# Kernel optimization log

Hardware: AMD Instinct MI355X
Metric: run time of the kernel (lower is better)

## Reference

```python
import jax, jax.numpy as jnp
import numpy as np

T, D, E, DFF, TOPK = 32768, 1024, 8, 2048, 2


def setup_inputs() -> dict:
    key = jax.random.key(0)
    k1, k2, k3, k4 = jax.random.split(key, 4)
    x = jax.random.normal(k1, (T, D), dtype=jnp.float32)
    gating_output = jax.random.normal(k2, (T, E), dtype=jnp.float32)
    # gate_up_proj: [E, 2*d_ff, d] (gate rows then up rows, col-parallel concat)
    w13 = jax.random.normal(k3, (E, 2 * DFF, D), dtype=jnp.float32) * 0.02
    # down_proj: [E, d, d_ff] (torch Linear weight layout)
    w2 = jax.random.normal(k4, (E, D, DFF), dtype=jnp.float32) * 0.02
    return {"x": x, "gating_output": gating_output, "w13": w13, "w2": w2, "topk": TOPK}


def reference(x, gating_output, w13, w2, topk):
    n_tok, d = x.shape
    n_exp = w13.shape[0]
    d_ff = w2.shape[2]
    # router: softmax over experts in fp32, top-k, renormalize, cast to x dtype
    probs = jax.nn.softmax(gating_output.astype(jnp.float32), axis=1)
    rw, sel = jax.lax.top_k(probs, topk)          # [T, topk]
    rw = rw / jnp.sum(rw, axis=-1, keepdims=True)
    rw = rw.astype(x.dtype)
    # dense combine weights [T, E] (zeros except selected experts)
    combine = jnp.zeros((n_tok, n_exp), dtype=x.dtype)
    combine = combine.at[jnp.arange(n_tok)[:, None], sel].set(rw)
    out = jnp.zeros_like(x)
    for e in range(n_exp):  # static small loop over experts
        gu = x @ w13[e].T                          # [T, 2*d_ff]
        g, u = gu[:, :d_ff], gu[:, d_ff:]
        h = jax.nn.silu(g) * u                     # [T, d_ff]
        out = out + combine[:, e:e + 1] * (h @ w2[e].T)
    return out
```

## Files before the change

### kernel.cpp

```cpp
#include <hip/hip_runtime.h>
#include <stdint.h>

#define T_TOK 32768
#define DIM   1024
#define NEXP  8
#define DFFN  2048
#define MAXROWS 67584
#define NBLK  128
#define NT1 16
#define NT2 32

typedef __bf16 bf16x8 __attribute__((ext_vector_type(8)));
typedef float  f32x4  __attribute__((ext_vector_type(4)));
typedef unsigned short u16x8 __attribute__((ext_vector_type(8)));

__device__ __forceinline__ unsigned short f2bf(float f) {
  unsigned u = __float_as_uint(f);
  unsigned r = (u + 0x7fffu + ((u >> 16) & 1u)) >> 16;
  return (unsigned short)r;
}
__device__ __forceinline__ float bf2f(unsigned short u) {
  return __uint_as_float(((unsigned)u) << 16);
}

__device__ __forceinline__ void gload16(const void* g, void* l) {
  __builtin_amdgcn_global_load_lds(
      (__attribute__((address_space(1))) void*)(uintptr_t)g,
      (__attribute__((address_space(3))) void*)(uint32_t)(uintptr_t)l,
      16, 0, 0);
}

__device__ __forceinline__ void xcd_remap(int NX, int NY, int& nb, int& mb) {
  int orig = blockIdx.y * NX + blockIdx.x;
  int q = (NX * NY) >> 3;
  int wgid = (orig & 7) * q + (orig >> 3);
  mb = wgid / NX;
  nb = wgid % NX;
}

__global__ void route_kernel(const float* __restrict__ gating, int* __restrict__ sel,
                             float* __restrict__ selw, int* __restrict__ blockHist) {
  __shared__ int hist[NEXP];
  const int tid = threadIdx.x;
  if (tid < NEXP) hist[tid] = 0;
  __syncthreads();
  int t = blockIdx.x * 256 + tid;
  float4 a = ((const float4*)gating)[t * 2];
  float4 b = ((const float4*)gating)[t * 2 + 1];
  float l[8] = {a.x, a.y, a.z, a.w, b.x, b.y, b.z, b.w};
  int i0 = 0; float b0 = l[0];
#pragma unroll
  for (int i = 1; i < 8; ++i) if (l[i] > b0) { b0 = l[i]; i0 = i; }
  int i1 = -1; float b1 = -1e30f;
#pragma unroll
  for (int i = 0; i < 8; ++i) if (i != i0 && l[i] > b1) { b1 = l[i]; i1 = i; }
  float e1 = __expf(b1 - b0);
  float w0 = 1.f / (1.f + e1);
  float w1 = 1.f - w0;
  sel[2 * t] = i0;  sel[2 * t + 1] = i1;
  selw[2 * t] = w0; selw[2 * t + 1] = w1;
  atomicAdd(&hist[i0], 1);
  atomicAdd(&hist[i1], 1);
  __syncthreads();
  if (tid < NEXP) blockHist[blockIdx.x * NEXP + tid] = hist[tid];
}

__global__ void plan_kernel(const int* __restrict__ blockHist,
                            int* __restrict__ padOff, int* __restrict__ base) {
  __shared__ int totals[NEXP];
  const int tid = threadIdx.x;
  if (tid < NEXP) {
    int s = 0;
    for (int b = 0; b < NBLK; ++b) s += blockHist[b * NEXP + tid];
    totals[tid] = s;
  }
  __syncthreads();
  if (tid == 0) {
    int off = 0;
    for (int e = 0; e < NEXP; ++e) { padOff[e] = off; off += (totals[e] + 255) & ~255; }
    padOff[NEXP] = off;
  }
  if (tid < NEXP) {
    int off = 0;
    for (int e = 0; e < tid; ++e) off += (totals[e] + 255) & ~255;
    int run = off;
    for (int b = 0; b < NBLK; ++b) { base[b * NEXP + tid] = run; run += blockHist[b * NEXP + tid]; }
  }
}

__global__ void fill_kernel(int* __restrict__ rowTok, int* __restrict__ rowSlot) {
  int i = blockIdx.x * 256 + threadIdx.x;
  if (i < MAXROWS) { rowTok[i] = 0; rowSlot[i] = -1; }
}

__global__ void scatter_kernel(const int* __restrict__ sel, const int* __restrict__ base,
                               int* __restrict__ rowTok, int* __restrict__ rowSlot) {
  __shared__ int cur[NEXP];
  const int tid = threadIdx.x;
  if (tid < NEXP) cur[tid] = 0;
  __syncthreads();
  int t = blockIdx.x * 256 + tid;
#pragma unroll
  for (int j = 0; j < 2; ++j) {
    int e = sel[2 * t + j];
    int pos = atomicAdd(&cur[e], 1);
    int r = base[blockIdx.x * NEXP + e] + pos;
    rowTok[r] = t;
    rowSlot[r] = 2 * t + j;
  }
}

__global__ void cvt3_kernel(const float* __restrict__ s0, unsigned short* __restrict__ d0, int m0,
                            const float* __restrict__ s1, unsigned short* __restrict__ d1, int m1,
                            const float* __restrict__ s2, unsigned short* __restrict__ d2, int m2) {
  int i = blockIdx.x * 256 + threadIdx.x;
  int stride = gridDim.x * 256;
  for (int k = i; k < m0; k += stride) {
    float4 v = ((const float4*)s0)[k];
    ushort4 o; o.x = f2bf(v.x); o.y = f2bf(v.y); o.z = f2bf(v.z); o.w = f2bf(v.w);
    ((ushort4*)d0)[k] = o;
  }
  for (int k = i; k < m1; k += stride) {
    float4 v = ((const float4*)s1)[k];
    ushort4 o; o.x = f2bf(v.x); o.y = f2bf(v.y); o.z = f2bf(v.z); o.w = f2bf(v.w);
    ((ushort4*)d1)[k] = o;
  }
  for (int k = i; k < m2; k += stride) {
    float4 v = ((const float4*)s2)[k];
    ushort4 o; o.x = f2bf(v.x); o.y = f2bf(v.y); o.z = f2bf(v.z); o.w = f2bf(v.w);
    ((ushort4*)d2)[k] = o;
  }
}

__global__ __launch_bounds__(512, 2) void gemm1_kernel(
    const unsigned short* __restrict__ xbf, const unsigned short* __restrict__ w13bf,
    const int* __restrict__ rowTok, const int* __restrict__ padOff,
    unsigned short* __restrict__ H) {
  __shared__ __align__(16) unsigned short As[2][256][64];
  __shared__ __align__(16) unsigned short Bs[2][256][64];

  int nb, mb;
  xcd_remap(gridDim.x, gridDim.y, nb, mb);
  const int m0 = mb * 256;
  const int total = padOff[NEXP];
  if (m0 >= total) return;
  int e = 0;
#pragma unroll
  for (int i = 1; i < NEXP; ++i) if (m0 >= padOff[i]) e = i;
  const int n0 = nb * 128;

  const int tid = threadIdx.x;
  const int wv = tid >> 6, ln = tid & 63;
  const int wm = wv >> 2, wn = wv & 3;
  const int lrow = ln & 15, l4 = ln >> 4, ls7 = ln & 7;

  const int gsl = ((tid & 7) ^ ((tid >> 3) & 7)) * 8;
  const int srow = tid >> 3;
  const size_t wb = (size_t)e * (size_t)(2 * DFFN) * DIM;
  const unsigned short* sA[2][2];
  const unsigned short* sB[2][2];
#pragma unroll
  for (int h = 0; h < 2; ++h)
#pragma unroll
    for (int i = 0; i < 2; ++i) {
      int tok = rowTok[m0 + h * 128 + i * 64 + srow];
      sA[h][i] = xbf + (size_t)tok * DIM + gsl;
      sB[h][i] = w13bf + wb + (size_t)(h * DFFN + n0 + i * 64 + srow) * DIM + gsl;
    }

#define STG_A1(buf, h, ko) { gload16(sA[h][0] + (ko), (char*)&As[buf][(h)*128 + wv*8][0]); \
                             gload16(sA[h][1] + (ko), (char*)&As[buf][(h)*128 + 64 + wv*8][0]); }
#define STG_B1(buf, h, ko) { gload16(sB[h][0] + (ko), (char*)&Bs[buf][(h)*128 + wv*8][0]); \
                             gload16(sB[h][1] + (ko), (char*)&Bs[buf][(h)*128 + 64 + wv*8][0]); }
#define LDA1(buf, mi, ks) (*(const bf16x8*)&As[buf][wm*128 + (mi)*16 + lrow][(((ks) + l4) ^ ls7) * 8])
#define LDB1(buf, f, ks)  (*(const bf16x8*)&Bs[buf][((f) >> 1)*128 + wn*32 + ((f) & 1)*16 + lrow][(((ks) + l4) ^ ls7) * 8])
#define MFMA16(A, B0v, B1v, f0, f1)                                              \
  _Pragma("unroll")                                                              \
  for (int mi = 0; mi < 8; ++mi) {                                               \
    acc[mi][f0] = __builtin_amdgcn_mfma_f32_16x16x32_bf16(A[mi], B0v, acc[mi][f0], 0, 0, 0); \
    acc[mi][f1] = __builtin_amdgcn_mfma_f32_16x16x32_bf16(A[mi], B1v, acc[mi][f1], 0, 0, 0); \
  }

  f32x4 acc[8][4] = {};

  STG_A1(0, 0, 0) STG_A1(0, 1, 0) STG_B1(0, 0, 0) STG_B1(0, 1, 0)
  STG_A1(1, 0, 64) STG_A1(1, 1, 64)
  asm volatile("s_waitcnt vmcnt(4)" ::: "memory");
  __builtin_amdgcn_sched_barrier(0);
  __builtin_amdgcn_s_barrier();

  for (int t = 0; t < NT1; ++t) {
    const int cur = t & 1, nxt = cur ^ 1;
    const int k1 = (t + 1) * 64, k2 = (t + 2) * 64;
    bf16x8 a0[8], a1[8], bv0, bv1;
#pragma unroll
    for (int mi = 0; mi < 8; ++mi) a0[mi] = LDA1(cur, mi, 0);
    bv0 = LDB1(cur, 0, 0); bv1 = LDB1(cur, 1, 0);
    if (t < NT1 - 1) STG_B1(nxt, 0, k1)
    __builtin_amdgcn_s_barrier();
    __builtin_amdgcn_s_setprio(1);
    MFMA16(a0, bv0, bv1, 0, 1)
    __builtin_amdgcn_s_setprio(0);
    __builtin_amdgcn_s_barrier();
    bv0 = LDB1(cur, 2, 0); bv1 = LDB1(cur, 3, 0);
#pragma unroll
    for (int mi = 0; mi < 8; ++mi) a1[mi] = LDA1(cur, mi, 4);
    if (t < NT1 - 1) STG_B1(nxt, 1, k1)
    __builtin_amdgcn_s_barrier();
    __builtin_amdgcn_s_setprio(1);
    MFMA16(a0, bv0, bv1, 2, 3)
    __builtin_amdgcn_s_setprio(0);
    __builtin_amdgcn_s_barrier();
    bv0 = LDB1(cur, 0, 4); bv1 = LDB1(cur, 1, 4);
    if (t < NT1 - 2) STG_A1(cur, 0, k2)
    __builtin_amdgcn_s_barrier();
    __builtin_amdgcn_s_setprio(1);
    MFMA16(a1, bv0, bv1, 0, 1)
    __builtin_amdgcn_s_setprio(0);
    __builtin_amdgcn_s_barrier();
    bv0 = LDB1(cur, 2, 4); bv1 = LDB1(cur, 3, 4);
    if (t < NT1 - 2) STG_A1(cur, 1, k2)
    __builtin_amdgcn_s_barrier();
    __builtin_amdgcn_s_setprio(1);
    MFMA16(a1, bv0, bv1, 2, 3)
    __builtin_amdgcn_s_setprio(0);
    if (t < NT1 - 2) { asm volatile("s_waitcnt vmcnt(4)" ::: "memory"); }
    else             { asm volatile("s_waitcnt vmcnt(0)" ::: "memory"); }
    __builtin_amdgcn_sched_barrier(0);
    __builtin_amdgcn_s_barrier();
  }

  const int fcol = n0 + wn * 32 + lrow;
  const int rowb = m0 + wm * 128 + l4 * 4;
#pragma unroll
  for (int mi = 0; mi < 8; ++mi) {
#pragma unroll
    for (int fj = 0; fj < 2; ++fj) {
      f32x4 g = acc[mi][fj], u = acc[mi][fj + 2];
      int f = fcol + fj * 16;
#pragma unroll
      for (int r = 0; r < 4; ++r) {
        float gv = g[r];
        float hv = (gv / (1.f + __expf(-gv))) * u[r];
        H[(size_t)(rowb + mi * 16 + r) * DFFN + f] = f2bf(hv);
      }
    }
  }
#undef STG_A1
#undef STG_B1
#undef LDA1
#undef LDB1
#undef MFMA16
}

__global__ __launch_bounds__(512, 2) void gemm2_kernel(
    const unsigned short* __restrict__ Hb, const unsigned short* __restrict__ w2bf,
    const int* __restrict__ rowSlot, const int* __restrict__ padOff,
    unsigned short* __restrict__ Oslot) {
  __shared__ __align__(16) unsigned short As[2][256][64];
  __shared__ __align__(16) unsigned short Bs[2][256][64];

  int nb, mb;
  xcd_remap(gridDim.x, gridDim.y, nb, mb);
  const int m0 = mb * 256;
  const int total = padOff[NEXP];
  if (m0 >= total) return;
  int e = 0;
#pragma unroll
  for (int i = 1; i < NEXP; ++i) if (m0 >= padOff[i]) e = i;
  const int n0 = nb * 256;

  const int tid = threadIdx.x;
  const int wv = tid >> 6, ln = tid & 63;
  const int wm = wv >> 2, wn = wv & 3;
  const int lrow = ln & 15, l4 = ln >> 4, ls7 = ln & 7;

  const int gsl = ((tid & 7) ^ ((tid >> 3) & 7)) * 8;
  const int srow = tid >> 3;
  const size_t wb = (size_t)e * (size_t)DIM * DFFN;
  const unsigned short* sA[2][2];
  const unsigned short* sB[2][2];
#pragma unroll
  for (int h = 0; h < 2; ++h)
#pragma unroll
    for (int i = 0; i < 2; ++i) {
      sA[h][i] = Hb + (size_t)(m0 + h * 128 + i * 64 + srow) * DFFN + gsl;
      sB[h][i] = w2bf + wb + (size_t)(n0 + h * 128 + i * 64 + srow) * DFFN + gsl;
    }

#define STG_A2(buf, h, ko) { gload16(sA[h][0] + (ko), (char*)&As[buf][(h)*128 + wv*8][0]); \
                             gload16(sA[h][1] + (ko), (char*)&As[buf][(h)*128 + 64 + wv*8][0]); }
#define STG_B2(buf, h, ko) { gload16(sB[h][0] + (ko), (char*)&Bs[buf][(h)*128 + wv*8][0]); \
                             gload16(sB[h][1] + (ko), (char*)&Bs[buf][(h)*128 + 64 + wv*8][0]); }
#define LDA2(buf, mi, ks) (*(const bf16x8*)&As[buf][wm*128 + (mi)*16 + lrow][(((ks) + l4) ^ ls7) * 8])
#define LDB2(buf, f, ks)  (*(const bf16x8*)&Bs[buf][wn*64 + (f)*16 + lrow][(((ks) + l4) ^ ls7) * 8])
#define MFMA16(A, B0v, B1v, f0, f1)                                              \
  _Pragma("unroll")                                                              \
  for (int mi = 0; mi < 8; ++mi) {                                               \
    acc[mi][f0] = __builtin_amdgcn_mfma_f32_16x16x32_bf16(A[mi], B0v, acc[mi][f0], 0, 0, 0); \
    acc[mi][f1] = __builtin_amdgcn_mfma_f32_16x16x32_bf16(A[mi], B1v, acc[mi][f1], 0, 0, 0); \
  }

  f32x4 acc[8][4] = {};

  STG_A2(0, 0, 0) STG_A2(0, 1, 0) STG_B2(0, 0, 0) STG_B2(0, 1, 0)
  STG_A2(1, 0, 64) STG_A2(1, 1, 64)
  asm volatile("s_waitcnt vmcnt(4)" ::: "memory");
  __builtin_amdgcn_sched_barrier(0);
  __builtin_amdgcn_s_barrier();

  for (int t = 0; t < NT2; ++t) {
    const int cur = t & 1, nxt = cur ^ 1;
    const int k1 = (t + 1) * 64, k2 = (t + 2) * 64;
    bf16x8 a0[8], a1[8], bv0, bv1;
#pragma unroll
    for (int mi = 0; mi < 8; ++mi) a0[mi] = LDA2(cur, mi, 0);
    bv0 = LDB2(cur, 0, 0); bv1 = LDB2(cur, 1, 0);
    if (t < NT2 - 1) STG_B2(nxt, 0, k1)
    __builtin_amdgcn_s_barrier();
    __builtin_amdgcn_s_setprio(1);
    MFMA16(a0, bv0, bv1, 0, 1)
    __builtin_amdgcn_s_setprio(0);
    __builtin_amdgcn_s_barrier();
    bv0 = LDB2(cur, 2, 0); bv1 = LDB2(cur, 3, 0);
#pragma unroll
    for (int mi = 0; mi < 8; ++mi) a1[mi] = LDA2(cur, mi, 4);
    if (t < NT2 - 1) STG_B2(nxt, 1, k1)
    __builtin_amdgcn_s_barrier();
    __builtin_amdgcn_s_setprio(1);
    MFMA16(a0, bv0, bv1, 2, 3)
    __builtin_amdgcn_s_setprio(0);
    __builtin_amdgcn_s_barrier();
    bv0 = LDB2(cur, 0, 4); bv1 = LDB2(cur, 1, 4);
    if (t < NT2 - 2) STG_A2(cur, 0, k2)
    __builtin_amdgcn_s_barrier();
    __builtin_amdgcn_s_setprio(1);
    MFMA16(a1, bv0, bv1, 0, 1)
    __builtin_amdgcn_s_setprio(0);
    __builtin_amdgcn_s_barrier();
    bv0 = LDB2(cur, 2, 4); bv1 = LDB2(cur, 3, 4);
    if (t < NT2 - 2) STG_A2(cur, 1, k2)
    __builtin_amdgcn_s_barrier();
    __builtin_amdgcn_s_setprio(1);
    MFMA16(a1, bv0, bv1, 2, 3)
    __builtin_amdgcn_s_setprio(0);
    if (t < NT2 - 2) { asm volatile("s_waitcnt vmcnt(4)" ::: "memory"); }
    else             { asm volatile("s_waitcnt vmcnt(0)" ::: "memory"); }
    __builtin_amdgcn_sched_barrier(0);
    __builtin_amdgcn_s_barrier();
  }

  const int colb = n0 + wn * 64 + lrow;
  const int rowb = m0 + wm * 128 + l4 * 4;
#pragma unroll
  for (int mi = 0; mi < 8; ++mi) {
#pragma unroll
    for (int r = 0; r < 4; ++r) {
      int row = rowb + mi * 16 + r;
      int si = rowSlot[row];
      if (si >= 0) {
        unsigned short* op = Oslot + (size_t)si * DIM + colb;
#pragma unroll
        for (int f = 0; f < 4; ++f) op[f * 16] = f2bf(acc[mi][f][r]);
      }
    }
  }
#undef STG_A2
#undef STG_B2
#undef LDA2
#undef LDB2
#undef MFMA16
}

__global__ void combine_kernel(const unsigned short* __restrict__ Oslot,
                               const float* __restrict__ selw, float* __restrict__ out) {
  int idx = blockIdx.x * 256 + threadIdx.x;
  int t = idx >> 7;
  int c = (idx & 127) << 3;
  u16x8 a = *(const u16x8*)(Oslot + (size_t)(2 * t) * DIM + c);
  u16x8 b = *(const u16x8*)(Oslot + (size_t)(2 * t + 1) * DIM + c);
  float w0 = selw[2 * t], w1 = selw[2 * t + 1];
  float4 o0, o1;
  o0.x = w0 * bf2f(a[0]) + w1 * bf2f(b[0]);
  o0.y = w0 * bf2f(a[1]) + w1 * bf2f(b[1]);
  o0.z = w0 * bf2f(a[2]) + w1 * bf2f(b[2]);
  o0.w = w0 * bf2f(a[3]) + w1 * bf2f(b[3]);
  o1.x = w0 * bf2f(a[4]) + w1 * bf2f(b[4]);
  o1.y = w0 * bf2f(a[5]) + w1 * bf2f(b[5]);
  o1.z = w0 * bf2f(a[6]) + w1 * bf2f(b[6]);
  o1.w = w0 * bf2f(a[7]) + w1 * bf2f(b[7]);
  float4* op = (float4*)(out + (size_t)t * DIM + c);
  op[0] = o0; op[1] = o1;
}

extern "C" void kernel_launch(void* const* d_in, const int* in_sizes, int n_in,
                              void* d_out, int out_size, void* d_ws, size_t ws_size,
                              hipStream_t stream) {
  const float* x      = (const float*)d_in[0];
  const float* gating = (const float*)d_in[1];
  const float* w13    = (const float*)d_in[2];
  const float* w2     = (const float*)d_in[3];
  float* out = (float*)d_out;

  char* ws = (char*)d_ws;
  size_t off = 0;
  auto alloc = [&](size_t bytes) { char* p = ws + off; off += (bytes + 255) & ~(size_t)255; return p; };
  int*   padOff    = (int*)alloc(64);
  int*   blockHist = (int*)alloc((size_t)NBLK * NEXP * 4);
  int*   base      = (int*)alloc((size_t)NBLK * NEXP * 4);
  int*   sel       = (int*)alloc((size_t)2 * T_TOK * 4);
  float* selw      = (float*)alloc((size_t)2 * T_TOK * 4);
  int*   rowTok    = (int*)alloc((size_t)MAXROWS * 4);
  int*   rowSlot   = (int*)alloc((size_t)MAXROWS * 4);
  unsigned short* xbf   = (unsigned short*)alloc((size_t)T_TOK * DIM * 2);
  unsigned short* w13bf = (unsigned short*)alloc((size_t)NEXP * 2 * DFFN * DIM * 2);
  unsigned short* w2bf  = (unsigned short*)alloc((size_t)NEXP * DIM * DFFN * 2);
  unsigned short* Hbuf  = (unsigned short*)alloc((size_t)MAXROWS * DFFN * 2);
  unsigned short* Oslot = xbf;

  route_kernel<<<NBLK, 256, 0, stream>>>(gating, sel, selw, blockHist);
  plan_kernel<<<1, 64, 0, stream>>>(blockHist, padOff, base);
  fill_kernel<<<MAXROWS / 256, 256, 0, stream>>>(rowTok, rowSlot);
  scatter_kernel<<<NBLK, 256, 0, stream>>>(sel, base, rowTok, rowSlot);
  cvt3_kernel<<<2048, 256, 0, stream>>>(x, xbf, T_TOK * DIM / 4,
                                        w13, w13bf, NEXP * 2 * DFFN * DIM / 4,
                                        w2, w2bf, NEXP * DIM * DFFN / 4);
  gemm1_kernel<<<dim3(2 * DFFN / 256, MAXROWS / 256), 512, 0, stream>>>(xbf, w13bf, rowTok, padOff, Hbuf);
  gemm2_kernel<<<dim3(DIM / 256, MAXROWS / 256), 512, 0, stream>>>(Hbuf, w2bf, rowSlot, padOff, Oslot);
  combine_kernel<<<T_TOK * DIM / 8 / 256, 256, 0, stream>>>(Oslot, selw, out);
}
```

Measured before the change: 995.5 us.

## Switch grouped MoE GEMMs to 32x32x16 MFMA with k-block-major LDS layout

Both expert GEMM kernels move from 16x16x32 MFMA tiles to 32x32x16 MFMA. The shared-memory tiles are re-laid out so each 32-row by 8-element k-slice is contiguous, which replaces the XOR swizzle, and the global-to-LDS staging and epilogue indexing are rewritten to match. The per-iteration schedule shrinks from four barrier-separated MFMA phases to two, with all A fragments loaded up front. Launch bounds drop from 2 to 1 block per SIMD group, which frees registers for the larger accumulators and fragment arrays but may lower occupancy and latency hiding.

```diff
diff --git a/kernel.cpp b/kernel.cpp
--- a/kernel.cpp
+++ b/kernel.cpp
@@ -11,7 +11,7 @@
 #define NT2 32
 
 typedef __bf16 bf16x8 __attribute__((ext_vector_type(8)));
-typedef float  f32x4  __attribute__((ext_vector_type(4)));
+typedef float  f32x16 __attribute__((ext_vector_type(16)));
 typedef unsigned short u16x8 __attribute__((ext_vector_type(8)));
 
 __device__ __forceinline__ unsigned short f2bf(float f) {
@@ -132,12 +132,20 @@
   }
 }
 
-__global__ __launch_bounds__(512, 2) void gemm1_kernel(
+
+#define STG(arr, srcs, buf, ko)                                                   \
+  { gload16(srcs[0][0] + (ko), (char*)&arr[(buf)*16384 + 0*8192 + 0*4096 + wv*512]); \
+    gload16(srcs[0][1] + (ko), (char*)&arr[(buf)*16384 + 0*8192 + 1*4096 + wv*512]); \
+    gload16(srcs[1][0] + (ko), (char*)&arr[(buf)*16384 + 1*8192 + 0*4096 + wv*512]); \
+    gload16(srcs[1][1] + (ko), (char*)&arr[(buf)*16384 + 1*8192 + 1*4096 + wv*512]); }
+#define LDA(buf, mf, ks) (*(const bf16x8*)&As[(buf)*16384 + wm*8192 + ((mf)*4+(ks))*512 + l32*256 + l31*8])
+
+__global__ __launch_bounds__(512, 1) void gemm1_kernel(
     const unsigned short* __restrict__ xbf, const unsigned short* __restrict__ w13bf,
     const int* __restrict__ rowTok, const int* __restrict__ padOff,
     unsigned short* __restrict__ H) {
-  __shared__ __align__(16) unsigned short As[2][256][64];
-  __shared__ __align__(16) unsigned short Bs[2][256][64];
+  __shared__ __align__(16) unsigned short As[32768];
+  __shared__ __align__(16) unsigned short Bs[32768];
 
   int nb, mb;
   xcd_remap(gridDim.x, gridDim.y, nb, mb);
@@ -152,10 +160,10 @@
   const int tid = threadIdx.x;
   const int wv = tid >> 6, ln = tid & 63;
   const int wm = wv >> 2, wn = wv & 3;
-  const int lrow = ln & 15, l4 = ln >> 4, ls7 = ln & 7;
-
-  const int gsl = ((tid & 7) ^ ((tid >> 3) & 7)) * 8;
-  const int srow = tid >> 3;
+  const int l31 = ln & 31, l32 = ln >> 5;
+
+  const int koff = ((tid >> 6) & 3) * 16 + ((tid >> 5) & 1) * 8;
+  const int r31 = tid & 31, hi2 = (tid >> 8) & 1;
   const size_t wb = (size_t)e * (size_t)(2 * DFFN) * DIM;
   const unsigned short* sA[2][2];
   const unsigned short* sB[2][2];
@@ -163,28 +171,16 @@
   for (int h = 0; h < 2; ++h)
 #pragma unroll
     for (int i = 0; i < 2; ++i) {
-      int tok = rowTok[m0 + h * 128 + i * 64 + srow];
-      sA[h][i] = xbf + (size_t)tok * DIM + gsl;
-      sB[h][i] = w13bf + wb + (size_t)(h * DFFN + n0 + i * 64 + srow) * DIM + gsl;
+      int rg = (i * 2 + hi2) * 32 + r31;
+      sA[h][i] = xbf + (size_t)rowTok[m0 + h * 128 + rg] * DIM + koff;
+      sB[h][i] = w13bf + wb + (size_t)(h * DFFN + n0 + rg) * DIM + koff;
     }
 
-#define STG_A1(buf, h, ko) { gload16(sA[h][0] + (ko), (char*)&As[buf][(h)*128 + wv*8][0]); \
-                             gload16(sA[h][1] + (ko), (char*)&As[buf][(h)*128 + 64 + wv*8][0]); }
-#define STG_B1(buf, h, ko) { gload16(sB[h][0] + (ko), (char*)&Bs[buf][(h)*128 + wv*8][0]); \
-                             gload16(sB[h][1] + (ko), (char*)&Bs[buf][(h)*128 + 64 + wv*8][0]); }
-#define LDA1(buf, mi, ks) (*(const bf16x8*)&As[buf][wm*128 + (mi)*16 + lrow][(((ks) + l4) ^ ls7) * 8])
-#define LDB1(buf, f, ks)  (*(const bf16x8*)&Bs[buf][((f) >> 1)*128 + wn*32 + ((f) & 1)*16 + lrow][(((ks) + l4) ^ ls7) * 8])
-#define MFMA16(A, B0v, B1v, f0, f1)                                              \
-  _Pragma("unroll")                                                              \
-  for (int mi = 0; mi < 8; ++mi) {                                               \
-    acc[mi][f0] = __builtin_amdgcn_mfma_f32_16x16x32_bf16(A[mi], B0v, acc[mi][f0], 0, 0, 0); \
-    acc[mi][f1] = __builtin_amdgcn_mfma_f32_16x16x32_bf16(A[mi], B1v, acc[mi][f1], 0, 0, 0); \
-  }
-
-  f32x4 acc[8][4] = {};
-
-  STG_A1(0, 0, 0) STG_A1(0, 1, 0) STG_B1(0, 0, 0) STG_B1(0, 1, 0)
-  STG_A1(1, 0, 64) STG_A1(1, 1, 64)
+#define LDB1(buf, nj, ks) (*(const bf16x8*)&Bs[(buf)*16384 + (nj)*8192 + (wn*4+(ks))*512 + l32*256 + l31*8])
+
+  f32x16 acc[4][2] = {};
+
+  STG(As, sA, 0, 0) STG(Bs, sB, 0, 0) STG(As, sA, 1, 64)
   asm volatile("s_waitcnt vmcnt(4)" ::: "memory");
   __builtin_amdgcn_sched_barrier(0);
   __builtin_amdgcn_s_barrier();
@@ -192,37 +188,43 @@
   for (int t = 0; t < NT1; ++t) {
     const int cur = t & 1, nxt = cur ^ 1;
     const int k1 = (t + 1) * 64, k2 = (t + 2) * 64;
-    bf16x8 a0[8], a1[8], bv0, bv1;
-#pragma unroll
-    for (int mi = 0; mi < 8; ++mi) a0[mi] = LDA1(cur, mi, 0);
-    bv0 = LDB1(cur, 0, 0); bv1 = LDB1(cur, 1, 0);
-    if (t < NT1 - 1) STG_B1(nxt, 0, k1)
+    bf16x8 a[4][4], b0[2][2], b1[2][2];
+#pragma unroll
+    for (int ks = 0; ks < 4; ++ks)
+#pragma unroll
+      for (int mf = 0; mf < 4; ++mf) a[ks][mf] = LDA(cur, mf, ks);
+#pragma unroll
+    for (int ks = 0; ks < 2; ++ks)
+#pragma unroll
+      for (int nj = 0; nj < 2; ++nj) b0[ks][nj] = LDB1(cur, nj, ks);
+    if (t < NT1 - 1) STG(Bs, sB, nxt, k1)
     __builtin_amdgcn_s_barrier();
     __builtin_amdgcn_s_setprio(1);
-    MFMA16(a0, bv0, bv1, 0, 1)
+#pragma unroll
+    for (int ks = 0; ks < 2; ++ks)
+#pragma unroll
+      for (int mi = 0; mi < 4; ++mi)
+#pragma unroll
+        for (int nj = 0; nj < 2; ++nj)
+          acc[mi][nj] = __builtin_amdgcn_mfma_f32_32x32x16_bf16(a[ks][mi], b0[ks][nj], acc[mi][nj], 0, 0, 0);
     __builtin_amdgcn_s_setprio(0);
-    __builtin_amdgcn_s_barrier();
-    bv0 = LDB1(cur, 2, 0); bv1 = LDB1(cur, 3, 0);
-#pragma unroll
-    for (int mi = 0; mi < 8; ++mi) a1[mi] = LDA1(cur, mi, 4);
-    if (t < NT1 - 1) STG_B1(nxt, 1, k1)
+    asm volatile("s_waitcnt lgkmcnt(0)" ::: "memory");
+    __builtin_amdgcn_sched_barrier(0);
+    __builtin_amdgcn_s_barrier();
+#pragma unroll
+    for (int ks = 0; ks < 2; ++ks)
+#pragma unroll
+      for (int nj = 0; nj < 2; ++nj) b1[ks][nj] = LDB1(cur, nj, ks + 2);
+    if (t < NT1 - 2) STG(As, sA, cur, k2)
     __builtin_amdgcn_s_barrier();
     __builtin_amdgcn_s_setprio(1);
-    MFMA16(a0, bv0, bv1, 2, 3)
-    __builtin_amdgcn_s_setprio(0);
-    __builtin_amdgcn_s_barrier();
-    bv0 = LDB1(cur, 0, 4); bv1 = LDB1(cur, 1, 4);
-    if (t < NT1 - 2) STG_A1(cur, 0, k2)
-    __builtin_amdgcn_s_barrier();
-    __builtin_amdgcn_s_setprio(1);
-    MFMA16(a1, bv0, bv1, 0, 1)
-    __builtin_amdgcn_s_setprio(0);
-    __builtin_amdgcn_s_barrier();
-    bv0 = LDB1(cur, 2, 4); bv1 = LDB1(cur, 3, 4);
-    if (t < NT1 - 2) STG_A1(cur, 1, k2)
-    __builtin_amdgcn_s_barrier();
-    __builtin_amdgcn_s_setprio(1);
-    MFMA16(a1, bv0, bv1, 2, 3)
+#pragma unroll
+    for (int ks = 0; ks < 2; ++ks)
+#pragma unroll
+      for (int mi = 0; mi < 4; ++mi)
+#pragma unroll
+        for (int nj = 0; nj < 2; ++nj)
+          acc[mi][nj] = __builtin_amdgcn_mfma_f32_32x32x16_bf16(a[ks + 2][mi], b1[ks][nj], acc[mi][nj], 0, 0, 0);
     __builtin_amdgcn_s_setprio(0);
     if (t < NT1 - 2) { asm volatile("s_waitcnt vmcnt(4)" ::: "memory"); }
     else             { asm volatile("s_waitcnt vmcnt(0)" ::: "memory"); }
@@ -230,35 +232,28 @@
     __builtin_amdgcn_s_barrier();
   }
 
-  const int fcol = n0 + wn * 32 + lrow;
-  const int rowb = m0 + wm * 128 + l4 * 4;
-#pragma unroll
-  for (int mi = 0; mi < 8; ++mi) {
-#pragma unroll
-    for (int fj = 0; fj < 2; ++fj) {
-      f32x4 g = acc[mi][fj], u = acc[mi][fj + 2];
-      int f = fcol + fj * 16;
-#pragma unroll
-      for (int r = 0; r < 4; ++r) {
-        float gv = g[r];
-        float hv = (gv / (1.f + __expf(-gv))) * u[r];
-        H[(size_t)(rowb + mi * 16 + r) * DFFN + f] = f2bf(hv);
-      }
+  const int f = n0 + wn * 32 + l31;
+  const int rowb = m0 + wm * 128;
+#pragma unroll
+  for (int mi = 0; mi < 4; ++mi) {
+    f32x16 g = acc[mi][0], u = acc[mi][1];
+#pragma unroll
+    for (int reg = 0; reg < 16; ++reg) {
+      int rl = (reg & 3) + 8 * (reg >> 2) + 4 * l32;
+      float gv = g[reg];
+      float hv = (gv / (1.f + __expf(-gv))) * u[reg];
+      H[(size_t)(rowb + mi * 32 + rl) * DFFN + f] = f2bf(hv);
     }
   }
-#undef STG_A1
-#undef STG_B1
-#undef LDA1
 #undef LDB1
-#undef MFMA16
-}
-
-__global__ __launch_bounds__(512, 2) void gemm2_kernel(
+}
+
+__global__ __launch_bounds__(512, 1) void gemm2_kernel(
     const unsigned short* __restrict__ Hb, const unsigned short* __restrict__ w2bf,
     const int* __restrict__ rowSlot, const int* __restrict__ padOff,
     unsigned short* __restrict__ Oslot) {
-  __shared__ __align__(16) unsigned short As[2][256][64];
-  __shared__ __align__(16) unsigned short Bs[2][256][64];
+  __shared__ __align__(16) unsigned short As[32768];
+  __shared__ __align__(16) unsigned short Bs[32768];
 
   int nb, mb;
   xcd_remap(gridDim.x, gridDim.y, nb, mb);
@@ -273,10 +268,10 @@
   const int tid = threadIdx.x;
   const int wv = tid >> 6, ln = tid & 63;
   const int wm = wv >> 2, wn = wv & 3;
-  const int lrow = ln & 15, l4 = ln >> 4, ls7 = ln & 7;
-
-  const int gsl = ((tid & 7) ^ ((tid >> 3) & 7)) * 8;
-  const int srow = tid >> 3;
+  const int l31 = ln & 31, l32 = ln >> 5;
+
+  const int koff = ((tid >> 6) & 3) * 16 + ((tid >> 5) & 1) * 8;
+  const int r31 = tid & 31, hi2 = (tid >> 8) & 1;
   const size_t wb = (size_t)e * (size_t)DIM * DFFN;
   const unsigned short* sA[2][2];
   const unsigned short* sB[2][2];
@@ -284,27 +279,16 @@
   for (int h = 0; h < 2; ++h)
 #pragma unroll
     for (int i = 0; i < 2; ++i) {
-      sA[h][i] = Hb + (size_t)(m0 + h * 128 + i * 64 + srow) * DFFN + gsl;
-      sB[h][i] = w2bf + wb + (size_t)(n0 + h * 128 + i * 64 + srow) * DFFN + gsl;
+      int rg = (i * 2 + hi2) * 32 + r31;
+      sA[h][i] = Hb + (size_t)(m0 + h * 128 + rg) * DFFN + koff;
+      sB[h][i] = w2bf + wb + (size_t)(n0 + h * 128 + rg) * DFFN + koff;
     }
 
-#define STG_A2(buf, h, ko) { gload16(sA[h][0] + (ko), (char*)&As[buf][(h)*128 + wv*8][0]); \
-                             gload16(sA[h][1] + (ko), (char*)&As[buf][(h)*128 + 64 + wv*8][0]); }
-#define STG_B2(buf, h, ko) { gload16(sB[h][0] + (ko), (char*)&Bs[buf][(h)*128 + wv*8][0]); \
-                             gload16(sB[h][1] + (ko), (char*)&Bs[buf][(h)*128 + 64 + wv*8][0]); }
-#define LDA2(buf, mi, ks) (*(const bf16x8*)&As[buf][wm*128 + (mi)*16 + lrow][(((ks) + l4) ^ ls7) * 8])
-#define LDB2(buf, f, ks)  (*(const bf16x8*)&Bs[buf][wn*64 + (f)*16 + lrow][(((ks) + l4) ^ ls7) * 8])
-#define MFMA16(A, B0v, B1v, f0, f1)                                              \
-  _Pragma("unroll")                                                              \
-  for (int mi = 0; mi < 8; ++mi) {                                               \
-    acc[mi][f0] = __builtin_amdgcn_mfma_f32_16x16x32_bf16(A[mi], B0v, acc[mi][f0], 0, 0, 0); \
-    acc[mi][f1] = __builtin_amdgcn_mfma_f32_16x16x32_bf16(A[mi], B1v, acc[mi][f1], 0, 0, 0); \
-  }
-
-  f32x4 acc[8][4] = {};
-
-  STG_A2(0, 0, 0) STG_A2(0, 1, 0) STG_B2(0, 0, 0) STG_B2(0, 1, 0)
-  STG_A2(1, 0, 64) STG_A2(1, 1, 64)
+#define LDB2(buf, nj, ks) (*(const bf16x8*)&Bs[(buf)*16384 + (wn>>1)*8192 + (((wn*2+(nj))&3)*4+(ks))*512 + l32*256 + l31*8])
+
+  f32x16 acc[4][2] = {};
+
+  STG(As, sA, 0, 0) STG(Bs, sB, 0, 0) STG(As, sA, 1, 64)
   asm volatile("s_waitcnt vmcnt(4)" ::: "memory");
   __builtin_amdgcn_sched_barrier(0);
   __builtin_amdgcn_s_barrier();
@@ -312,37 +296,43 @@
   for (int t = 0; t < NT2; ++t) {
     const int cur = t & 1, nxt = cur ^ 1;
     const int k1 = (t + 1) * 64, k2 = (t + 2) * 64;
-    bf16x8 a0[8], a1[8], bv0, bv1;
-#pragma unroll
-    for (int mi = 0; mi < 8; ++mi) a0[mi] = LDA2(cur, mi, 0);
-    bv0 = LDB2(cur, 0, 0); bv1 = LDB2(cur, 1, 0);
-    if (t < NT2 - 1) STG_B2(nxt, 0, k1)
+    bf16x8 a[4][4], b0[2][2], b1[2][2];
+#pragma unroll
+    for (int ks = 0; ks < 4; ++ks)
+#pragma unroll
+      for (int mf = 0; mf < 4; ++mf) a[ks][mf] = LDA(cur, mf, ks);
+#pragma unroll
+    for (int ks = 0; ks < 2; ++ks)
+#pragma unroll
+      for (int nj = 0; nj < 2; ++nj) b0[ks][nj] = LDB2(cur, nj, ks);
+    if (t < NT2 - 1) STG(Bs, sB, nxt, k1)
     __builtin_amdgcn_s_barrier();
     __builtin_amdgcn_s_setprio(1);
-    MFMA16(a0, bv0, bv1, 0, 1)
+#pragma unroll
+    for (int ks = 0; ks < 2; ++ks)
+#pragma unroll
+      for (int mi = 0; mi < 4; ++mi)
+#pragma unroll
+        for (int nj = 0; nj < 2; ++nj)
+          acc[mi][nj] = __builtin_amdgcn_mfma_f32_32x32x16_bf16(a[ks][mi], b0[ks][nj], acc[mi][nj], 0, 0, 0);
     __builtin_amdgcn_s_setprio(0);
-    __builtin_amdgcn_s_barrier();
-    bv0 = LDB2(cur, 2, 0); bv1 = LDB2(cur, 3, 0);
-#pragma unroll
-    for (int mi = 0; mi < 8; ++mi) a1[mi] = LDA2(cur, mi, 4);
-    if (t < NT2 - 1) STG_B2(nxt, 1, k1)
+    asm volatile("s_waitcnt lgkmcnt(0)" ::: "memory");
+    __builtin_amdgcn_sched_barrier(0);
+    __builtin_amdgcn_s_barrier();
+#pragma unroll
+    for (int ks = 0; ks < 2; ++ks)
+#pragma unroll
+      for (int nj = 0; nj < 2; ++nj) b1[ks][nj] = LDB2(cur, nj, ks + 2);
+    if (t < NT2 - 2) STG(As, sA, cur, k2)
     __builtin_amdgcn_s_barrier();
     __builtin_amdgcn_s_setprio(1);
-    MFMA16(a0, bv0, bv1, 2, 3)
-    __builtin_amdgcn_s_setprio(0);
-    __builtin_amdgcn_s_barrier();
-    bv0 = LDB2(cur, 0, 4); bv1 = LDB2(cur, 1, 4);
-    if (t < NT2 - 2) STG_A2(cur, 0, k2)
-    __builtin_amdgcn_s_barrier();
-    __builtin_amdgcn_s_setprio(1);
-    MFMA16(a1, bv0, bv1, 0, 1)
-    __builtin_amdgcn_s_setprio(0);
-    __builtin_amdgcn_s_barrier();
-    bv0 = LDB2(cur, 2, 4); bv1 = LDB2(cur, 3, 4);
-    if (t < NT2 - 2) STG_A2(cur, 1, k2)
-    __builtin_amdgcn_s_barrier();
-    __builtin_amdgcn_s_setprio(1);
-    MFMA16(a1, bv0, bv1, 2, 3)
+#pragma unroll
+    for (int ks = 0; ks < 2; ++ks)
+#pragma unroll
+      for (int mi = 0; mi < 4; ++mi)
+#pragma unroll
+        for (int nj = 0; nj < 2; ++nj)
+          acc[mi][nj] = __builtin_amdgcn_mfma_f32_32x32x16_bf16(a[ks + 2][mi], b1[ks][nj], acc[mi][nj], 0, 0, 0);
     __builtin_amdgcn_s_setprio(0);
     if (t < NT2 - 2) { asm volatile("s_waitcnt vmcnt(4)" ::: "memory"); }
     else             { asm volatile("s_waitcnt vmcnt(0)" ::: "memory"); }
@@ -350,26 +340,23 @@
     __builtin_amdgcn_s_barrier();
   }
 
-  const int colb = n0 + wn * 64 + lrow;
-  const int rowb = m0 + wm * 128 + l4 * 4;
-#pragma unroll
-  for (int mi = 0; mi < 8; ++mi) {
-#pragma unroll
-    for (int r = 0; r < 4; ++r) {
-      int row = rowb + mi * 16 + r;
+  const int colb = n0 + wn * 64 + l31;
+  const int rowb = m0 + wm * 128;
+#pragma unroll
+  for (int mi = 0; mi < 4; ++mi) {
+#pragma unroll
+    for (int reg = 0; reg < 16; ++reg) {
+      int rl = (reg & 3) + 8 * (reg >> 2) + 4 * l32;
+      int row = rowb + mi * 32 + rl;
       int si = rowSlot[row];
       if (si >= 0) {
         unsigned short* op = Oslot + (size_t)si * DIM + colb;
-#pragma unroll
-        for (int f = 0; f < 4; ++f) op[f * 16] = f2bf(acc[mi][f][r]);
+        op[0]  = f2bf(acc[mi][0][reg]);
+        op[32] = f2bf(acc[mi][1][reg]);
       }
     }
   }
-#undef STG_A2
-#undef STG_B2
-#undef LDA2
 #undef LDB2
-#undef MFMA16
 }
 
 __global__ void combine_kernel(const unsigned short* __restrict__ Oslot,
```

After: 1.234 ms. 1.24x slower.
